# Kernel optimization log

Hardware: AMD Instinct MI355X
Metric: run time of the kernel (lower is better)

## Reference

```python
import jax, jax.numpy as jnp
import numpy as np
from jax import lax


def _pixel_shuffle2(y):
    # torch.nn.PixelShuffle(2): (B, C*4, H, W) -> (B, C, 2H, 2W)
    B, C4, H, W = y.shape
    C = C4 // 4
    y = y.reshape(B, C, 2, 2, H, W)
    y = y.transpose(0, 1, 4, 2, 5, 3)  # B, C, H, r, W, r
    return y.reshape(B, C, H * 2, W * 2)


def setup_inputs() -> dict:
    key = jax.random.key(0)
    k1, k2, k3 = jax.random.split(key, 3)
    n_feat = 96
    x = jax.random.normal(k1, (8, n_feat, 128, 128), dtype=jnp.float32)
    # Conv2d(n_feat, n_feat*2, 3, bias=False); fan-in scaled init
    conv_w = jax.random.normal(k2, (n_feat * 2, n_feat, 3, 3), dtype=jnp.float32) * (1.0 / np.sqrt(n_feat * 9))
    beta = jnp.float32(0.3)
    return {"x": x, "conv_w": conv_w, "beta": beta}


def reference(x, conv_w, beta):
    # conv 3x3 stride 1 pad 1, no bias
    y = lax.conv_general_dilated(
        x, conv_w, window_strides=(1, 1), padding=((1, 1), (1, 1)),
        dimension_numbers=("NCHW", "OIHW", "NCHW"))
    y = _pixel_shuffle2(y)  # (B, n_feat/2, 2H, 2W)
    H2, W2 = y.shape[2], y.shape[3]
    # forward-normalized 2D FFT; torch fftshift with no dim shifts ALL axes
    freq = jnp.fft.fftshift(jnp.fft.fft2(y.astype(jnp.complex64), norm="forward"))
    # crop central low-frequency band (half-size in each spatial dim)
    low = freq[:, :, H2 // 4: H2 // 4 * 3, W2 // 4: W2 // 4 * 3]
    # F.pad(low, (H2//4, H2//4, W2//4, W2//4)): last dim padded by H2//4, dim -2 by W2//4
    low = jnp.pad(low, ((0, 0), (0, 0), (W2 // 4, W2 // 4), (H2 // 4, H2 // 4)))
    low = jnp.abs(jnp.fft.ifft2(jnp.fft.ifftshift(low), norm="forward")).astype(x.dtype)
    high = y - low
    return (1.0 - beta) * low + beta * high
```

## Files before the change

### kernel.cpp

```cpp
#include <hip/hip_runtime.h>
#include <math.h>

#define PI_F 3.14159265358979f

typedef __attribute__((ext_vector_type(8))) __bf16 bf16x8;
typedef __attribute__((ext_vector_type(4))) float f32x4;

__device__ __forceinline__ unsigned short f2bf_rne(float v) {
  union { float f; unsigned u; } c; c.f = v;
  unsigned u = c.u;
  return (unsigned short)((u + 0x7fffu + ((u >> 16) & 1u)) >> 16);
}
__device__ __forceinline__ float bfbits2f(unsigned short b) {
  union { unsigned u; float f; } c; c.u = ((unsigned)b) << 16; return c.f;
}

__global__ void prep_w(const float* __restrict__ w, unsigned short* __restrict__ whi,
                       unsigned short* __restrict__ wlo) {
  int i = blockIdx.x * 256 + threadIdx.x;
  if (i >= 9 * 192 * 96) return;
  int pos = i / (192 * 96);
  int rem = i - pos * (192 * 96);
  float v = w[(size_t)rem * 9 + pos];
  unsigned short h = f2bf_rne(v);
  whi[i] = h;
  wlo[i] = f2bf_rne(v - bfbits2f(h));
}

#define ICP 104

__global__ __launch_bounds__(256)
void conv_mfma(const float* __restrict__ x,
               const unsigned short* __restrict__ whi, const unsigned short* __restrict__ wlo,
               float* __restrict__ y) {
  __shared__ unsigned short patch[3 * 66 * ICP];
  const int tid  = threadIdx.x;
  const int wave = tid >> 6, lane = tid & 63;
  const int col  = lane & 15, quad = lane >> 4;
  const int w0 = blockIdx.x * 64;
  const int h  = blockIdx.y;
  const int b  = blockIdx.z;
  const float* xb = x + (size_t)b * 96 * 128 * 128;

  {
    const int l16 = tid & 15;
    const int pg  = tid >> 4;
#pragma unroll
    for (int it = 0; it < 18; ++it) {
      int pp = it * 16 + pg;
      int r  = pp % 3;
      int ic = pp / 3;
      int gr = h - 1 + r;
      const float* rowp = xb + (size_t)ic * 16384 + gr * 128;
      float4 v = make_float4(0.f, 0.f, 0.f, 0.f);
      if ((unsigned)gr < 128u) v = *(const float4*)(rowp + w0 + 4 * l16);
      unsigned short* pb = &patch[(r * 66 + 1 + 4 * l16) * ICP + ic];
      pb[0]       = f2bf_rne(v.x);
      pb[ICP]     = f2bf_rne(v.y);
      pb[2 * ICP] = f2bf_rne(v.z);
      pb[3 * ICP] = f2bf_rne(v.w);
      if (l16 < 2) {
        int gc = (l16 == 0) ? (w0 - 1) : (w0 + 64);
        float hv = 0.f;
        if ((unsigned)gr < 128u && (unsigned)gc < 128u) hv = rowp[gc];
        patch[(r * 66 + (l16 == 0 ? 0 : 65)) * ICP + ic] = f2bf_rne(hv);
      }
    }
  }
  __syncthreads();

  f32x4 acc[3][4];
#pragma unroll
  for (int mt = 0; mt < 3; ++mt)
#pragma unroll
    for (int nt = 0; nt < 4; ++nt) acc[mt][nt] = (f32x4)0.f;

  for (int pos = 0; pos < 9; ++pos) {
    const int dy = pos / 3, dx = pos - 3 * (pos / 3);
#pragma unroll
    for (int icc = 0; icc < 96; icc += 32) {
      bf16x8 bfrag[4];
#pragma unroll
      for (int nt = 0; nt < 4; ++nt) {
        int px = nt * 16 + col;
        bfrag[nt] = *(const bf16x8*)&patch[(dy * 66 + px + dx) * ICP + icc + quad * 8];
      }
#pragma unroll
      for (int mt = 0; mt < 3; ++mt) {
        int oc = 48 * wave + mt * 16 + col;
        size_t o = (size_t)pos * 18432 + (size_t)oc * 96 + icc + quad * 8;
        bf16x8 ah = *(const bf16x8*)(whi + o);
        bf16x8 al = *(const bf16x8*)(wlo + o);
#pragma unroll
        for (int nt = 0; nt < 4; ++nt) {
          acc[mt][nt] = __builtin_amdgcn_mfma_f32_16x16x32_bf16(ah, bfrag[nt], acc[mt][nt], 0, 0, 0);
          acc[mt][nt] = __builtin_amdgcn_mfma_f32_16x16x32_bf16(al, bfrag[nt], acc[mt][nt], 0, 0, 0);
        }
      }
    }
  }

  float* yb = y + (size_t)b * 48 * 65536;
#pragma unroll
  for (int mt = 0; mt < 3; ++mt) {
#pragma unroll
    for (int r = 0; r < 4; ++r) {
      int oc = 48 * wave + mt * 16 + quad * 4 + r;
      int cq = oc >> 2, r2 = (oc >> 1) & 1, s2 = oc & 1;
      float* orow = yb + ((size_t)cq * 256 + 2 * h + r2) * 256;
#pragma unroll
      for (int nt = 0; nt < 4; ++nt) {
        int w = w0 + nt * 16 + col;
        orow[2 * w + s2] = acc[mt][nt][r];
      }
    }
  }
}

#define OCB 8
#define ICB 2
#define PSTRIDE 67
__global__ __launch_bounds__(256)
void conv_ps_kernel(const float* __restrict__ x, const float* __restrict__ wgt,
                    float* __restrict__ y) {
  __shared__ float wsh[OCB * 96 * 9];
  __shared__ float patch[ICB * 18 * PSTRIDE];
  const int tid = threadIdx.x;
  const int b = blockIdx.z / 24, ocg = blockIdx.z % 24;
  const int row0 = blockIdx.y * 16, col0 = blockIdx.x * 64;
  const int tx = tid & 15, ty = tid >> 4;
  for (int i = tid; i < OCB * 96 * 9; i += 256) wsh[i] = wgt[ocg * (OCB * 96 * 9) + i];
  float acc[OCB][4];
#pragma unroll
  for (int o = 0; o < OCB; ++o)
#pragma unroll
    for (int p = 0; p < 4; ++p) acc[o][p] = 0.f;
  const float* xb = x + (size_t)b * 96 * 128 * 128;
  for (int ic0 = 0; ic0 < 96; ic0 += ICB) {
    __syncthreads();
    for (int idx = tid; idx < ICB * 18 * 66; idx += 256) {
      int j = idx / (18 * 66), rem = idx - j * (18 * 66);
      int r = rem / 66, c = rem - r * 66;
      int gr = row0 - 1 + r, gc = col0 - 1 + c;
      float v = 0.f;
      if ((unsigned)gr < 128u && (unsigned)gc < 128u)
        v = xb[((size_t)(ic0 + j) * 128 + gr) * 128 + gc];
      patch[j * (18 * PSTRIDE) + r * PSTRIDE + c] = v;
    }
    __syncthreads();
#pragma unroll
    for (int j = 0; j < ICB; ++j) {
      float xr[3][6];
      const float* pp = &patch[j * (18 * PSTRIDE) + ty * PSTRIDE + tx * 4];
#pragma unroll
      for (int dy = 0; dy < 3; ++dy)
#pragma unroll
        for (int dx = 0; dx < 6; ++dx) xr[dy][dx] = pp[dy * PSTRIDE + dx];
#pragma unroll
      for (int o = 0; o < OCB; ++o) {
        const float* wp = &wsh[(o * 96 + ic0 + j) * 9];
#pragma unroll
        for (int p = 0; p < 4; ++p)
          acc[o][p] += wp[0] * xr[0][p] + wp[1] * xr[0][p + 1] + wp[2] * xr[0][p + 2]
                     + wp[3] * xr[1][p] + wp[4] * xr[1][p + 1] + wp[5] * xr[1][p + 2]
                     + wp[6] * xr[2][p] + wp[7] * xr[2][p + 1] + wp[8] * xr[2][p + 2];
      }
    }
  }
  const int h = row0 + ty;
#pragma unroll
  for (int o = 0; o < OCB; ++o) {
    int ocglob = ocg * OCB + o;
    int cq = ocglob >> 2, r2 = (ocglob >> 1) & 1, s2 = ocglob & 1;
    float* orow = y + (((size_t)b * 48 + cq) * 256 + (2 * h + r2)) * 256;
#pragma unroll
    for (int p = 0; p < 4; ++p) orow[2 * (col0 + tx * 4 + p) + s2] = acc[o][p];
  }
}

__device__ __forceinline__ float2 cadd(float2 a, float2 b){return make_float2(a.x+b.x, a.y+b.y);}
__device__ __forceinline__ float2 csub(float2 a, float2 b){return make_float2(a.x-b.x, a.y-b.y);}
__device__ __forceinline__ float2 cmul(float2 a, float2 b){return make_float2(a.x*b.x-a.y*b.y, a.x*b.y+a.y*b.x);}
__device__ __forceinline__ float2 cmulc(float2 a, float2 b){return make_float2(a.x*b.x+a.y*b.y, a.y*b.x-a.x*b.y);}

__device__ __forceinline__ void dft4(float2 r[4]) {
  float2 e0 = cadd(r[0], r[2]), e1 = csub(r[0], r[2]);
  float2 o0 = cadd(r[1], r[3]), o1 = csub(r[1], r[3]);
  r[0] = cadd(e0, o0);
  r[2] = csub(e0, o0);
  r[1] = make_float2(e1.x + o1.y, e1.y - o1.x);
  r[3] = make_float2(e1.x - o1.y, e1.y + o1.x);
}
__device__ __forceinline__ void idft4(float2 r[4]) {
  float2 e0 = cadd(r[0], r[2]), e1 = csub(r[0], r[2]);
  float2 o0 = cadd(r[1], r[3]), o1 = csub(r[1], r[3]);
  r[0] = cadd(e0, o0);
  r[2] = csub(e0, o0);
  r[1] = make_float2(e1.x - o1.y, e1.y + o1.x);
  r[3] = make_float2(e1.x + o1.y, e1.y - o1.x);
}

struct TwSet {
  float2 f1[3], f2[3], f3[3], i2[4], i3[4];
};

__device__ __forceinline__ void load_tw(TwSet& T, const float2* __restrict__ tw, int l) {
  const int qq = l >> 4, m = l & 15, q2r = (l >> 2) & 3, c2 = l & 3;
  T.f1[0] = tw[l];
  T.f1[1] = tw[(2 * l) & 255];
  T.f1[2] = tw[(3 * l) & 255];
  T.f2[0] = tw[(4 * m) & 255];
  T.f2[1] = tw[(8 * m) & 255];
  T.f2[2] = tw[(12 * m) & 255];
  T.f3[0] = tw[(16 * c2) & 255];
  T.f3[1] = tw[(32 * c2) & 255];
  T.f3[2] = tw[(48 * c2) & 255];
  T.i2[0] = tw[(4 * c2 * q2r) & 255];
  T.i2[1] = tw[(4 * (c2 + 4) * q2r) & 255];
  T.i2[2] = tw[(4 * (c2 + 8) * q2r) & 255];
  T.i2[3] = tw[(4 * (c2 + 12) * q2r) & 255];
  T.i3[0] = tw[(m * qq) & 255];
  T.i3[1] = tw[((m + 16) * qq) & 255];
  T.i3[2] = tw[((m + 32) * qq) & 255];
  T.i3[3] = tw[((m + 48) * qq) & 255];
}

template <int ST>
__device__ void fft_line_masked(float2 r[4], float2* __restrict__ S, const TwSet& T, int l) {
  const int qq = l >> 4, m = l & 15;
  const int g = l >> 2, q2r = (l >> 2) & 3, c2 = l & 3;
  dft4(r);
  r[1] = cmul(r[1], T.f1[0]);
  r[2] = cmul(r[2], T.f1[1]);
  r[3] = cmul(r[3], T.f1[2]);
  S[ST * l] = r[0];
  S[ST * (64 + l)] = r[1];
  S[ST * (128 + l)] = r[2];
  S[ST * (192 + l)] = r[3];
#pragma unroll
  for (int t = 0; t < 4; ++t) r[t] = S[ST * (qq * 64 + m + 16 * t)];
  dft4(r);
  r[1] = cmul(r[1], T.f2[0]);
  r[2] = cmul(r[2], T.f2[1]);
  r[3] = cmul(r[3], T.f2[2]);
#pragma unroll
  for (int q2 = 0; q2 < 4; ++q2) S[ST * (qq * 64 + q2 * 16 + ((m + 4 * q2) & 15))] = r[q2];
#pragma unroll
  for (int t = 0; t < 4; ++t) r[t] = S[ST * (qq * 64 + q2r * 16 + ((c2 + 4 * t + 4 * q2r) & 15))];
  dft4(r);
  r[1] = cmul(r[1], T.f3[0]);
  r[2] = cmul(r[2], T.f3[1]);
  r[3] = cmul(r[3], T.f3[2]);
#pragma unroll
  for (int q3 = 0; q3 < 4; ++q3) S[ST * (g * 16 + ((4 * q3 + c2 + g) & 15))] = r[q3];
#pragma unroll
  for (int t = 0; t < 4; ++t) r[t] = S[ST * (g * 16 + ((4 * c2 + t + g) & 15))];
  dft4(r);
  {
    float2 V0 = r[0], V3 = r[3];
    r[0] = cadd(V0, V3);
    r[1] = make_float2(V0.x + V3.y, V0.y - V3.x);
    r[2] = csub(V0, V3);
    r[3] = make_float2(V0.x - V3.y, V0.y + V3.x);
  }
  r[1] = cmulc(r[1], T.f3[0]);
  r[2] = cmulc(r[2], T.f3[1]);
  r[3] = cmulc(r[3], T.f3[2]);
#pragma unroll
  for (int j = 0; j < 4; ++j) S[ST * (g * 16 + ((4 * c2 + j + g) & 15))] = r[j];
#pragma unroll
  for (int t = 0; t < 4; ++t) r[t] = S[ST * (g * 16 + ((4 * t + c2 + g) & 15))];
  idft4(r);
  r[0] = cmulc(r[0], T.i2[0]);
  r[1] = cmulc(r[1], T.i2[1]);
  r[2] = cmulc(r[2], T.i2[2]);
  r[3] = cmulc(r[3], T.i2[3]);
#pragma unroll
  for (int t1 = 0; t1 < 4; ++t1) S[ST * (qq * 64 + q2r * 16 + ((c2 + 4 * t1 + 4 * q2r) & 15))] = r[t1];
#pragma unroll
  for (int t = 0; t < 4; ++t) r[t] = S[ST * (qq * 64 + t * 16 + ((m + 4 * t) & 15))];
  idft4(r);
  r[0] = cmulc(r[0], T.i3[0]);
  r[1] = cmulc(r[1], T.i3[1]);
  r[2] = cmulc(r[2], T.i3[2]);
  r[3] = cmulc(r[3], T.i3[3]);
#pragma unroll
  for (int t2 = 0; t2 < 4; ++t2) S[ST * (qq * 64 + m + 16 * t2)] = r[t2];
#pragma unroll
  for (int t = 0; t < 4; ++t) r[t] = S[ST * (t * 64 + l)];
  idft4(r);
}

__global__ __launch_bounds__(256)
void fft_rows_kernel(const float* __restrict__ y, float2* __restrict__ z1) {
  __shared__ float2 S[4 * 256];
  __shared__ float2 tw[256];
  const int tid = threadIdx.x;
  {
    float sn, cs;
    __sincosf(-2.f * PI_F * (float)tid / 256.f, &sn, &cs);
    tw[tid] = make_float2(cs, sn);
  }
  __syncthreads();
  const int wv = tid >> 6, l = tid & 63;
  TwSet T;
  load_tw(T, tw, l);
  const size_t rowbase = ((size_t)blockIdx.x * 4 + wv) * 256;
  float2 r[4];
#pragma unroll
  for (int t = 0; t < 4; ++t) r[t] = make_float2(y[rowbase + l + 64 * t], 0.f);
  fft_line_masked<1>(r, S + wv * 256, T, l);
#pragma unroll
  for (int t = 0; t < 4; ++t)
    z1[rowbase + l + 64 * t] = make_float2(r[t].x * (1.f / 256.f), r[t].y * (1.f / 256.f));
}

#define CST 17
__global__ __launch_bounds__(256)
void fft_cols_kernel(const float2* __restrict__ z1, const float* __restrict__ yy,
                     float* __restrict__ out, const float* __restrict__ betaPtr) {
  __shared__ float2 strip[256 * CST];
  __shared__ float2 tw[256];
  const int tid = threadIdx.x;
  {
    float sn, cs;
    __sincosf(-2.f * PI_F * (float)tid / 256.f, &sn, &cs);
    tw[tid] = make_float2(cs, sn);
  }
  const int img = blockIdx.x >> 4;
  const int c0 = (blockIdx.x & 15) * 16;
  const size_t ibase = (size_t)img * 65536;
#pragma unroll
  for (int it = 0; it < 16; ++it) {
    int idx = it * 256 + tid;
    int rrow = idx >> 4, cc = idx & 15;
    strip[rrow * CST + cc] = z1[ibase + (size_t)rrow * 256 + c0 + cc];
  }
  __syncthreads();
  const int wv = tid >> 6, l = tid & 63;
  TwSet T;
  load_tw(T, tw, l);
  float2 r[4];
#pragma unroll
  for (int ci = 0; ci < 4; ++ci) {
    const int c = wv * 4 + ci;
    float2* Sc = strip + c;
#pragma unroll
    for (int t = 0; t < 4; ++t) r[t] = Sc[CST * (l + 64 * t)];
    fft_line_masked<CST>(r, Sc, T, l);
#pragma unroll
    for (int t = 0; t < 4; ++t) {
      float2 v = r[t];
      Sc[CST * (l + 64 * t)].x = sqrtf(v.x * v.x + v.y * v.y) * (1.f / 256.f);
    }
  }
  __syncthreads();
  const float beta = betaPtr[0];
  const float a1 = 1.f - 2.f * beta;
#pragma unroll
  for (int it = 0; it < 16; ++it) {
    int idx = it * 256 + tid;
    int rrow = idx >> 4, cc = idx & 15;
    size_t gi = ibase + (size_t)rrow * 256 + c0 + cc;
    out[gi] = beta * yy[gi] + a1 * strip[rrow * CST + cc].x;
  }
}

extern "C" void kernel_launch(void* const* d_in, const int* in_sizes, int n_in,
                              void* d_out, int out_size, void* d_ws, size_t ws_size,
                              hipStream_t stream) {
  const float* x = (const float*)d_in[0];
  const float* wgt = (const float*)d_in[1];
  const float* beta = (const float*)d_in[2];
  float* out = (float*)d_out;

  const size_t wplane = (size_t)9 * 192 * 96;
  const size_t wbytes = (2 * wplane * sizeof(unsigned short) + 255) & ~(size_t)255;
  const size_t per_img = 65536ull * sizeof(float2);
  const int NIMG = 8 * 48;

  float2* z1;
  size_t z1_bytes;

  if (ws_size >= wbytes + per_img) {
    unsigned short* whi = (unsigned short*)d_ws;
    unsigned short* wlo = whi + wplane;
    z1 = (float2*)((char*)d_ws + wbytes);
    z1_bytes = ws_size - wbytes;
    prep_w<<<648, 256, 0, stream>>>(wgt, whi, wlo);
    conv_mfma<<<dim3(2, 128, 8), 256, 0, stream>>>(x, whi, wlo, out);
  } else {
    z1 = (float2*)d_ws;
    z1_bytes = ws_size;
    conv_ps_kernel<<<dim3(2, 8, 192), 256, 0, stream>>>(x, wgt, out);
  }

  int chunk = (int)(z1_bytes / per_img);
  if (chunk < 1) chunk = 1;
  if (chunk > NIMG) chunk = NIMG;
  for (int img0 = 0; img0 < NIMG; img0 += chunk) {
    int n = NIMG - img0;
    if (n > chunk) n = chunk;
    float* ych = out + (size_t)img0 * 65536;
    fft_rows_kernel<<<n * 64, 256, 0, stream>>>(ych, z1);
    fft_cols_kernel<<<n * 16, 256, 0, stream>>>(z1, ych, ych, beta);
  }
}
```

Before: 436.7 us.

## Interleave bf16 hi/lo weights, double-buffer weight loads, vectorize patch and output stores

```diff
diff --git a/kernel.cpp b/kernel.cpp
--- a/kernel.cpp
+++ b/kernel.cpp
@@ -14,24 +14,29 @@
 __device__ __forceinline__ float bfbits2f(unsigned short b) {
   union { unsigned u; float f; } c; c.u = ((unsigned)b) << 16; return c.f;
 }
-
-__global__ void prep_w(const float* __restrict__ w, unsigned short* __restrict__ whi,
-                       unsigned short* __restrict__ wlo) {
+__device__ __forceinline__ unsigned pk2(float a, float b) {
+  return (unsigned)f2bf_rne(a) | ((unsigned)f2bf_rne(b) << 16);
+}
+
+__global__ void prep_w(const float* __restrict__ w, unsigned short* __restrict__ wpk) {
   int i = blockIdx.x * 256 + threadIdx.x;
   if (i >= 9 * 192 * 96) return;
   int pos = i / (192 * 96);
   int rem = i - pos * (192 * 96);
+  int oc = rem / 96, ic = rem - oc * 96;
   float v = w[(size_t)rem * 9 + pos];
   unsigned short h = f2bf_rne(v);
-  whi[i] = h;
-  wlo[i] = f2bf_rne(v - bfbits2f(h));
+  unsigned short l = f2bf_rne(v - bfbits2f(h));
+  int q = ic >> 3, j = ic & 7;
+  size_t base = ((size_t)(pos * 192 + oc) * 12 + q) * 16;
+  wpk[base + j] = h;
+  wpk[base + 8 + j] = l;
 }
 
 #define ICP 104
 
-__global__ __launch_bounds__(256)
-void conv_mfma(const float* __restrict__ x,
-               const unsigned short* __restrict__ whi, const unsigned short* __restrict__ wlo,
+__global__ __launch_bounds__(256, 3)
+void conv_mfma(const float* __restrict__ x, const unsigned short* __restrict__ wpk,
                float* __restrict__ y) {
   __shared__ unsigned short patch[3 * 66 * ICP];
   const int tid  = threadIdx.x;
@@ -43,28 +48,34 @@
   const float* xb = x + (size_t)b * 96 * 128 * 128;
 
   {
-    const int l16 = tid & 15;
-    const int pg  = tid >> 4;
-#pragma unroll
-    for (int it = 0; it < 18; ++it) {
-      int pp = it * 16 + pg;
-      int r  = pp % 3;
-      int ic = pp / 3;
+    const int cg = tid & 15, pg = tid >> 4;
+#pragma unroll
+    for (int it = 0; it < 9; ++it) {
+      int pairid = it * 16 + pg;
+      int r  = pairid % 3;
+      int ic = (pairid / 3) * 2;
       int gr = h - 1 + r;
-      const float* rowp = xb + (size_t)ic * 16384 + gr * 128;
-      float4 v = make_float4(0.f, 0.f, 0.f, 0.f);
-      if ((unsigned)gr < 128u) v = *(const float4*)(rowp + w0 + 4 * l16);
-      unsigned short* pb = &patch[(r * 66 + 1 + 4 * l16) * ICP + ic];
-      pb[0]       = f2bf_rne(v.x);
-      pb[ICP]     = f2bf_rne(v.y);
-      pb[2 * ICP] = f2bf_rne(v.z);
-      pb[3 * ICP] = f2bf_rne(v.w);
-      if (l16 < 2) {
-        int gc = (l16 == 0) ? (w0 - 1) : (w0 + 64);
-        float hv = 0.f;
-        if ((unsigned)gr < 128u && (unsigned)gc < 128u) hv = rowp[gc];
-        patch[(r * 66 + (l16 == 0 ? 0 : 65)) * ICP + ic] = f2bf_rne(hv);
+      const float* r0p = xb + (size_t)ic * 16384 + gr * 128 + w0 + 4 * cg;
+      float4 v0 = make_float4(0.f, 0.f, 0.f, 0.f), v1 = v0;
+      if ((unsigned)gr < 128u) {
+        v0 = *(const float4*)(r0p);
+        v1 = *(const float4*)(r0p + 16384);
       }
+      unsigned* pb = (unsigned*)&patch[(r * 66 + 1 + 4 * cg) * ICP + ic];
+      pb[0]           = pk2(v0.x, v1.x);
+      pb[ICP / 2]     = pk2(v0.y, v1.y);
+      pb[ICP]         = pk2(v0.z, v1.z);
+      pb[3 * ICP / 2] = pk2(v0.w, v1.w);
+    }
+    for (int idx = tid; idx < 576; idx += 256) {
+      int side = idx & 1, pr = idx >> 1;
+      int r = pr % 3, ic = pr / 3;
+      int gr = h - 1 + r;
+      int gc = side ? (w0 + 64) : (w0 - 1);
+      float v = 0.f;
+      if ((unsigned)gr < 128u && (unsigned)gc < 128u)
+        v = xb[(size_t)ic * 16384 + gr * 128 + gc];
+      patch[(r * 66 + (side ? 65 : 0)) * ICP + ic] = f2bf_rne(v);
     }
   }
   __syncthreads();
@@ -75,43 +86,51 @@
 #pragma unroll
     for (int nt = 0; nt < 4; ++nt) acc[mt][nt] = (f32x4)0.f;
 
-  for (int pos = 0; pos < 9; ++pos) {
-    const int dy = pos / 3, dx = pos - 3 * (pos / 3);
-#pragma unroll
-    for (int icc = 0; icc < 96; icc += 32) {
-      bf16x8 bfrag[4];
+  const int wbase = (48 * wave + col) * 192 + quad * 16;
+
+  bf16x8 ah[2][3], al[2][3];
+  auto WLD = [&](int ST, int SL) {
+#pragma unroll
+    for (int mt = 0; mt < 3; ++mt) {
+      const unsigned short* wp_ =
+          wpk + wbase + (((ST / 3) * 192 + mt * 16) * 12 + (ST % 3) * 4) * 16;
+      ah[SL][mt] = *(const bf16x8*)(wp_);
+      al[SL][mt] = *(const bf16x8*)(wp_ + 8);
+    }
+  };
+
+  WLD(0, 0);
+#pragma unroll
+  for (int st = 0; st < 27; ++st) {
+    const int sl = st & 1;
+    if (st < 26) WLD(st + 1, sl ^ 1);
+    const int pos = st / 3, dy = pos / 3, dx = pos - 3 * dy, icc = (st % 3) * 32;
+    bf16x8 bfrag[4];
+#pragma unroll
+    for (int nt = 0; nt < 4; ++nt)
+      bfrag[nt] = *(const bf16x8*)&patch[(dy * 66 + nt * 16 + col + dx) * ICP + icc + quad * 8];
+#pragma unroll
+    for (int mt = 0; mt < 3; ++mt)
 #pragma unroll
       for (int nt = 0; nt < 4; ++nt) {
-        int px = nt * 16 + col;
-        bfrag[nt] = *(const bf16x8*)&patch[(dy * 66 + px + dx) * ICP + icc + quad * 8];
+        acc[mt][nt] = __builtin_amdgcn_mfma_f32_16x16x32_bf16(ah[sl][mt], bfrag[nt], acc[mt][nt], 0, 0, 0);
+        acc[mt][nt] = __builtin_amdgcn_mfma_f32_16x16x32_bf16(al[sl][mt], bfrag[nt], acc[mt][nt], 0, 0, 0);
       }
-#pragma unroll
-      for (int mt = 0; mt < 3; ++mt) {
-        int oc = 48 * wave + mt * 16 + col;
-        size_t o = (size_t)pos * 18432 + (size_t)oc * 96 + icc + quad * 8;
-        bf16x8 ah = *(const bf16x8*)(whi + o);
-        bf16x8 al = *(const bf16x8*)(wlo + o);
-#pragma unroll
-        for (int nt = 0; nt < 4; ++nt) {
-          acc[mt][nt] = __builtin_amdgcn_mfma_f32_16x16x32_bf16(ah, bfrag[nt], acc[mt][nt], 0, 0, 0);
-          acc[mt][nt] = __builtin_amdgcn_mfma_f32_16x16x32_bf16(al, bfrag[nt], acc[mt][nt], 0, 0, 0);
-        }
-      }
-    }
   }
 
   float* yb = y + (size_t)b * 48 * 65536;
 #pragma unroll
   for (int mt = 0; mt < 3; ++mt) {
 #pragma unroll
-    for (int r = 0; r < 4; ++r) {
-      int oc = 48 * wave + mt * 16 + quad * 4 + r;
-      int cq = oc >> 2, r2 = (oc >> 1) & 1, s2 = oc & 1;
+    for (int p = 0; p < 2; ++p) {
+      int r0 = 2 * p;
+      int oc = 48 * wave + mt * 16 + quad * 4 + r0;
+      int cq = oc >> 2, r2 = (oc >> 1) & 1;
       float* orow = yb + ((size_t)cq * 256 + 2 * h + r2) * 256;
 #pragma unroll
       for (int nt = 0; nt < 4; ++nt) {
         int w = w0 + nt * 16 + col;
-        orow[2 * w + s2] = acc[mt][nt][r];
+        *(float2*)&orow[2 * w] = make_float2(acc[mt][nt][r0], acc[mt][nt][r0 + 1]);
       }
     }
   }
@@ -383,12 +402,11 @@
   size_t z1_bytes;
 
   if (ws_size >= wbytes + per_img) {
-    unsigned short* whi = (unsigned short*)d_ws;
-    unsigned short* wlo = whi + wplane;
+    unsigned short* wpk = (unsigned short*)d_ws;
     z1 = (float2*)((char*)d_ws + wbytes);
     z1_bytes = ws_size - wbytes;
-    prep_w<<<648, 256, 0, stream>>>(wgt, whi, wlo);
-    conv_mfma<<<dim3(2, 128, 8), 256, 0, stream>>>(x, whi, wlo, out);
+    prep_w<<<648, 256, 0, stream>>>(wgt, wpk);
+    conv_mfma<<<dim3(2, 128, 8), 256, 0, stream>>>(x, wpk, out);
   } else {
     z1 = (float2*)d_ws;
     z1_bytes = ws_size;
```

After: 472.7 us. +8.2%, slower.
